# Kernel tuning notes

Measured on AMD Instinct MI355X. Metric: run time of the kernel, lower is better.

## Reference

```python
import jax, jax.numpy as jnp
import numpy as np

B, IN, OUT, ORDER = 8192, 1024, 1024, 7


def setup_inputs() -> dict:
    key = jax.random.key(0)
    k1, k2 = jax.random.split(key)
    x = jax.random.normal(k1, (B, IN), dtype=jnp.float32)
    tanh_range = jnp.float32(1.0)
    coef = jax.random.normal(k2, (OUT, IN, ORDER + 1), dtype=jnp.float32) * 0.1
    return {"x": x, "tanh_range": tanh_range, "coef": coef}


def _poly(x, tanh_range, order):
    # t^0, t^1, ..., t^order via cumulative products (matches torch recurrence)
    t = jnp.tanh(x * tanh_range)                      # [B, IN]
    powers = jnp.cumprod(jnp.broadcast_to(t[..., None], t.shape + (order,)), axis=-1)
    ones = jnp.ones_like(t)[..., None]
    return jnp.concatenate([ones, powers], axis=-1)   # [B, IN, order+1]


def reference(x, tanh_range, coef):
    poly = _poly(x, tanh_range, ORDER)                # [B, IN, K]
    # output[b, j] = sum_{i,k} coef[j,i,k] * poly[b,i,k]
    return jnp.einsum('bik,jik->bj', poly, coef)
```

## Files before the change

### kernel.cpp

```cpp
#include <hip/hip_runtime.h>
#include <hip/hip_bf16.h>


#define BM 128
#define BN 128
#define BK 128
#define KT 7168
#define KFULL 8192

typedef short bf16x8 __attribute__((ext_vector_type(8)));
typedef short bf16x4 __attribute__((ext_vector_type(4)));
typedef float f32x4  __attribute__((ext_vector_type(4)));

__device__ __forceinline__ unsigned short f2bf(float f) {
    union { float f; unsigned u; } v; v.f = f;
    unsigned r = v.u + 0x7fffu + ((v.u >> 16) & 1u);
    return (unsigned short)(r >> 16);
}

__device__ __forceinline__ void gload_lds16(const void* gp, void* lp) {
    __builtin_amdgcn_global_load_lds(
        (const __attribute__((address_space(1))) void*)gp,
        (__attribute__((address_space(3))) void*)lp, 16, 0, 0);
}

#define CVT_BLOCKS  512
#define TANH_BLOCKS 4096

__global__ __launch_bounds__(256)
void prep(const float* __restrict__ x, const float* __restrict__ trp,
          const float* __restrict__ coef, unsigned short* __restrict__ coef_bf,
          unsigned short* __restrict__ A, float* __restrict__ bias) {
    __shared__ unsigned short st[256 * 56];
    __shared__ float redbuf[4];

    const int t   = threadIdx.x;
    const int blk = blockIdx.x;
    const int rl  = t >> 7;
    const int ig  = t & 127;
    const bool is_cvt = (blk < CVT_BLOCKS);

    unsigned short tmp[56];

    if (is_cvt) {
        const int j = blk * 2 + rl;
        const float* src = coef + (size_t)j * KFULL + ig * 64;
        float k0sum = 0.f;
        #pragma unroll
        for (int i = 0; i < 8; ++i) {
            const float4 f0 = *(const float4*)(src + i * 8);
            const float4 f1 = *(const float4*)(src + i * 8 + 4);
            k0sum += f0.x;
            tmp[i*7+0] = f2bf(f0.y); tmp[i*7+1] = f2bf(f0.z); tmp[i*7+2] = f2bf(f0.w);
            tmp[i*7+3] = f2bf(f1.x); tmp[i*7+4] = f2bf(f1.y);
            tmp[i*7+5] = f2bf(f1.z); tmp[i*7+6] = f2bf(f1.w);
        }
        #pragma unroll
        for (int off = 32; off > 0; off >>= 1) k0sum += __shfl_down(k0sum, off, 64);
        if ((t & 63) == 0) redbuf[t >> 6] = k0sum;
    } else {
        const int bb = (blk - CVT_BLOCKS) * 2 + rl;
        const float tr = trp[0];
        const float* xp = x + (size_t)bb * 1024 + ig * 8;
        const float4 x0 = *(const float4*)xp;
        const float4 x1 = *(const float4*)(xp + 4);
        const float xs[8] = {x0.x, x0.y, x0.z, x0.w, x1.x, x1.y, x1.z, x1.w};
        #pragma unroll
        for (int i = 0; i < 8; ++i) {
            const float e  = __expf(2.0f * tr * xs[i]);
            const float tt = 1.0f - 2.0f * __builtin_amdgcn_rcpf(e + 1.0f);
            float pw = tt;
            #pragma unroll
            for (int k = 1; k < 8; ++k) { tmp[i * 7 + k - 1] = f2bf(pw); pw *= tt; }
        }
    }

    #pragma unroll
    for (int v = 0; v < 7; ++v)
        *(bf16x8*)&st[t * 56 + v * 8] = *(bf16x8*)&tmp[v * 8];

    __syncthreads();

    if (is_cvt) {
        if (t == 0)   bias[blk * 2]     = redbuf[0] + redbuf[1];
        if (t == 128) bias[blk * 2 + 1] = redbuf[2] + redbuf[3];
    }

    unsigned short* dstbase = is_cvt
        ? coef_bf + (size_t)(blk * 2) * KT
        : A       + (size_t)((blk - CVT_BLOCKS) * 2) * KT;
    #pragma unroll
    for (int v = 0; v < 7; ++v) {
        const int c   = v * 256 + t;
        const int row = c / 896;
        const int cc  = c - row * 896;
        const int igs = cc / 7;
        const int q   = cc - igs * 7;
        const bf16x8 pk = *(const bf16x8*)&st[(row * 128 + igs) * 56 + q * 8];
        *(bf16x8*)(dstbase + (size_t)c * 8) = pk;
    }
}

__global__ __launch_bounds__(256, 2)
void gemm_bt(const unsigned short* __restrict__ A, const unsigned short* __restrict__ Bt,
             const float* __restrict__ bias, float* __restrict__ out)
{
    __shared__ unsigned short As[BM * BK];
    __shared__ unsigned short Bs[BN * BK];

    const int t    = threadIdx.x;
    const int m0   = blockIdx.x * BM;
    const int n0   = blockIdx.y * BN;
    const int w    = t >> 6;
    const int lane = t & 63;
    const int wm   = (w >> 1) * 64;
    const int wn   = (w & 1) * 64;
    const int lrow = lane & 15;

    const int srow   = t >> 4;
    const int schunk = (t & 15) ^ srow;
    const int wbase  = w * 512;

    f32x4 acc[4][4];
    #pragma unroll
    for (int i = 0; i < 4; i++)
        #pragma unroll
        for (int j = 0; j < 4; j++)
            acc[i][j] = (f32x4){0.f, 0.f, 0.f, 0.f};

    const size_t abase = (size_t)(m0 + srow) * KT + schunk * 8;
    const size_t bbase = (size_t)(n0 + srow) * KT + schunk * 8;

    for (int k0 = 0; k0 < KT; k0 += BK) {
        #pragma unroll
        for (int r = 0; r < 8; ++r)
            gload_lds16(A + abase + (size_t)r * 16 * KT + k0, &As[r * 2048 + wbase]);
        #pragma unroll
        for (int r = 0; r < 8; ++r)
            gload_lds16(Bt + bbase + (size_t)r * 16 * KT + k0, &Bs[r * 2048 + wbase]);

        __syncthreads();

        #pragma unroll
        for (int kk = 0; kk < BK; kk += 32) {
            const int soff = ((((kk >> 3) + (lane >> 4)) ^ (lane & 15)) * 8);
            bf16x8 a[4], b[4];
            #pragma unroll
            for (int i = 0; i < 4; i++)
                a[i] = *(const bf16x8*)&As[(wm + i * 16 + lrow) * BK + soff];
            #pragma unroll
            for (int j = 0; j < 4; j++)
                b[j] = *(const bf16x8*)&Bs[(wn + j * 16 + lrow) * BK + soff];
            #pragma unroll
            for (int i = 0; i < 4; i++)
                #pragma unroll
                for (int j = 0; j < 4; j++)
                    acc[i][j] = __builtin_amdgcn_mfma_f32_16x16x32_bf16(a[i], b[j], acc[i][j], 0, 0, 0);
        }

        __syncthreads();
    }

    const int crow = (lane >> 4) * 4;
    const int ccol = lane & 15;
    #pragma unroll
    for (int j = 0; j < 4; j++) {
        const int n = n0 + wn + j * 16 + ccol;
        const float bv = bias[n];
        #pragma unroll
        for (int i = 0; i < 4; i++) {
            const int m = m0 + wm + i * 16 + crow;
            #pragma unroll
            for (int r = 0; r < 4; ++r)
                out[(size_t)(m + r) * 1024 + n] = acc[i][j][r] + bv;
        }
    }
}

#define LDK 72
__global__ __launch_bounds__(256, 2)
void taylor_gemm(const float* __restrict__ x, const float* __restrict__ trp,
                 const float* __restrict__ coef, float* __restrict__ out)
{
    __shared__ unsigned short As[BM * LDK];
    __shared__ unsigned short Bs[BN * LDK];

    const int t  = threadIdx.x;
    const int m0 = blockIdx.x * BM;
    const int n0 = blockIdx.y * BN;
    const float tr = trp[0];

    const int w    = t >> 6;
    const int lane = t & 63;
    const int wm   = (w >> 1) * 64;
    const int wn   = (w & 1) * 64;
    const int lrow = lane & 15;
    const int kq   = (lane >> 4) * 8;

    f32x4 acc[4][4];
    #pragma unroll
    for (int i = 0; i < 4; i++)
        #pragma unroll
        for (int j = 0; j < 4; j++)
            acc[i][j] = (f32x4){0.f, 0.f, 0.f, 0.f};

    const int bcol  = t & 15;
    const int brow0 = t >> 4;
    const int acol  = t & 7;
    const int arow0 = t >> 3;

    for (int k0 = 0; k0 < KFULL; k0 += 64) {
        const int i0 = k0 >> 3;
        #pragma unroll
        for (int r = 0; r < 8; ++r) {
            const int row = brow0 + r * 16;
            const float4 v = *(const float4*)(coef + (size_t)(n0 + row) * KFULL + k0 + bcol * 4);
            bf16x4 pk;
            pk[0] = (short)f2bf(v.x); pk[1] = (short)f2bf(v.y);
            pk[2] = (short)f2bf(v.z); pk[3] = (short)f2bf(v.w);
            *(bf16x4*)&Bs[row * LDK + bcol * 4] = pk;
        }
        #pragma unroll
        for (int r = 0; r < 4; ++r) {
            const int row = arow0 + r * 32;
            const float xv = x[(size_t)(m0 + row) * 1024 + i0 + acol];
            const float e  = __expf(2.0f * tr * xv);
            const float tt = 1.0f - 2.0f / (e + 1.0f);
            bf16x8 pk;
            float p = 1.0f;
            #pragma unroll
            for (int k = 0; k < 8; ++k) { pk[k] = (short)f2bf(p); p *= tt; }
            *(bf16x8*)&As[row * LDK + acol * 8] = pk;
        }
        __syncthreads();
        #pragma unroll
        for (int kk = 0; kk < 64; kk += 32) {
            bf16x8 a[4], b[4];
            #pragma unroll
            for (int i = 0; i < 4; i++)
                a[i] = *(const bf16x8*)&As[(wm + i * 16 + lrow) * LDK + kk + kq];
            #pragma unroll
            for (int j = 0; j < 4; j++)
                b[j] = *(const bf16x8*)&Bs[(wn + j * 16 + lrow) * LDK + kk + kq];
            #pragma unroll
            for (int i = 0; i < 4; i++)
                #pragma unroll
                for (int j = 0; j < 4; j++)
                    acc[i][j] = __builtin_amdgcn_mfma_f32_16x16x32_bf16(a[i], b[j], acc[i][j], 0, 0, 0);
        }
        __syncthreads();
    }

    const int crow = (lane >> 4) * 4;
    const int ccol = lane & 15;
    #pragma unroll
    for (int i = 0; i < 4; i++) {
        #pragma unroll
        for (int j = 0; j < 4; j++) {
            const int m = m0 + wm + i * 16 + crow;
            const int n = n0 + wn + j * 16 + ccol;
            #pragma unroll
            for (int r = 0; r < 4; ++r)
                out[(size_t)(m + r) * 1024 + n] = acc[i][j][r];
        }
    }
}

extern "C" void kernel_launch(void* const* d_in, const int* in_sizes, int n_in,
                              void* d_out, int out_size, void* d_ws, size_t ws_size,
                              hipStream_t stream) {
    const float* x    = (const float*)d_in[0];
    const float* trp  = (const float*)d_in[1];
    const float* coef = (const float*)d_in[2];
    float* out = (float*)d_out;

    const size_t A_BYTES    = (size_t)8192 * KT * 2;
    const size_t COEF_BYTES = (size_t)1024 * KT * 2;
    const size_t BIAS_BYTES = 1024 * sizeof(float);
    dim3 block(256);

    if (ws_size >= A_BYTES + COEF_BYTES + BIAS_BYTES) {
        unsigned short* A_bf    = (unsigned short*)d_ws;
        unsigned short* coef_bf = (unsigned short*)((char*)d_ws + A_BYTES);
        float*          bias    = (float*)((char*)d_ws + A_BYTES + COEF_BYTES);

        prep<<<dim3(CVT_BLOCKS + TANH_BLOCKS), block, 0, stream>>>(
            x, trp, coef, coef_bf, A_bf, bias);
        gemm_bt<<<dim3(8192 / BM, 1024 / BN), block, 0, stream>>>(
            A_bf, coef_bf, bias, out);
    } else {
        taylor_gemm<<<dim3(8192 / BM, 1024 / BN), block, 0, stream>>>(x, trp, coef, out);
    }
}
```

Measured before the change: 229.3 us.

## Rewrite bf16 GEMM with 256x128 tiles, triple-buffered async loads and split barriers

```diff
diff --git a/kernel.cpp b/kernel.cpp
--- a/kernel.cpp
+++ b/kernel.cpp
@@ -2,11 +2,18 @@
 #include <hip/hip_bf16.h>
 
 
+#define KT 7168
+#define KFULL 8192
+
+#define TM 256
+#define TN 128
+#define TK 64
+#define NTILES (KT / TK)
+#define BUF_USH 24576
+#define BOFF 16384
+
 #define BM 128
 #define BN 128
-#define BK 128
-#define KT 7168
-#define KFULL 8192
 
 typedef short bf16x8 __attribute__((ext_vector_type(8)));
 typedef short bf16x4 __attribute__((ext_vector_type(4)));
@@ -23,6 +30,12 @@
         (const __attribute__((address_space(1))) void*)gp,
         (__attribute__((address_space(3))) void*)lp, 16, 0, 0);
 }
+
+#define BARRIER() do { \
+    asm volatile("" ::: "memory"); \
+    __builtin_amdgcn_s_barrier(); \
+    asm volatile("" ::: "memory"); \
+} while (0)
 
 #define CVT_BLOCKS  512
 #define TANH_BLOCKS 4096
@@ -101,25 +114,29 @@
     }
 }
 
-__global__ __launch_bounds__(256, 2)
+__global__ __launch_bounds__(512, 2)
 void gemm_bt(const unsigned short* __restrict__ A, const unsigned short* __restrict__ Bt,
              const float* __restrict__ bias, float* __restrict__ out)
 {
-    __shared__ unsigned short As[BM * BK];
-    __shared__ unsigned short Bs[BN * BK];
+    __shared__ unsigned short lds[3 * BUF_USH];
 
     const int t    = threadIdx.x;
-    const int m0   = blockIdx.x * BM;
-    const int n0   = blockIdx.y * BN;
+    const int m0   = blockIdx.x * TM;
+    const int n0   = blockIdx.y * TN;
     const int w    = t >> 6;
     const int lane = t & 63;
     const int wm   = (w >> 1) * 64;
     const int wn   = (w & 1) * 64;
     const int lrow = lane & 15;
-
-    const int srow   = t >> 4;
-    const int schunk = (t & 15) ^ srow;
-    const int wbase  = w * 512;
+    const int lq   = lane >> 4;
+
+    const int S = ((lq ^ (lane & 7)) << 3);
+
+    const int srow = t >> 3;
+    const int schk = (t & 7) ^ (srow & 7);
+    const size_t aGbase = (size_t)(m0 + srow) * KT + schk * 8;
+    const size_t bGbase = (size_t)(n0 + srow) * KT + schk * 8;
+    const int wofs = w * 512;
 
     f32x4 acc[4][4];
     #pragma unroll
@@ -128,37 +145,97 @@
         for (int j = 0; j < 4; j++)
             acc[i][j] = (f32x4){0.f, 0.f, 0.f, 0.f};
 
-    const size_t abase = (size_t)(m0 + srow) * KT + schunk * 8;
-    const size_t bbase = (size_t)(n0 + srow) * KT + schunk * 8;
-
-    for (int k0 = 0; k0 < KT; k0 += BK) {
-        #pragma unroll
-        for (int r = 0; r < 8; ++r)
-            gload_lds16(A + abase + (size_t)r * 16 * KT + k0, &As[r * 2048 + wbase]);
-        #pragma unroll
-        for (int r = 0; r < 8; ++r)
-            gload_lds16(Bt + bbase + (size_t)r * 16 * KT + k0, &Bs[r * 2048 + wbase]);
-
-        __syncthreads();
-
-        #pragma unroll
-        for (int kk = 0; kk < BK; kk += 32) {
-            const int soff = ((((kk >> 3) + (lane >> 4)) ^ (lane & 15)) * 8);
-            bf16x8 a[4], b[4];
-            #pragma unroll
-            for (int i = 0; i < 4; i++)
-                a[i] = *(const bf16x8*)&As[(wm + i * 16 + lrow) * BK + soff];
-            #pragma unroll
-            for (int j = 0; j < 4; j++)
-                b[j] = *(const bf16x8*)&Bs[(wn + j * 16 + lrow) * BK + soff];
-            #pragma unroll
-            for (int i = 0; i < 4; i++)
+    #pragma unroll
+    for (int s = 0; s < 4; ++s)
+        gload_lds16(A + aGbase + (size_t)(s * 64) * KT, &lds[s * 4096 + wofs]);
+    #pragma unroll
+    for (int s = 0; s < 2; ++s)
+        gload_lds16(Bt + bGbase + (size_t)(s * 64) * KT, &lds[BOFF + s * 4096 + wofs]);
+    #pragma unroll
+    for (int s = 0; s < 4; ++s)
+        gload_lds16(A + aGbase + (size_t)(s * 64) * KT + TK, &lds[BUF_USH + s * 4096 + wofs]);
+    #pragma unroll
+    for (int s = 0; s < 2; ++s)
+        gload_lds16(Bt + bGbase + (size_t)(s * 64) * KT + TK, &lds[BUF_USH + BOFF + s * 4096 + wofs]);
+
+    asm volatile("s_waitcnt vmcnt(6)" ::: "memory");
+    BARRIER();
+
+    int bufR = 0;
+    int bufW = 2 * BUF_USH;
+
+    for (int kt = 0; kt < NTILES; ++kt) {
+        const int  k2 = (kt + 2) * TK;
+        const bool pf = (kt + 2 < NTILES);
+
+        bf16x8 b0[4][2], a0[2][2];
+        #pragma unroll
+        for (int j = 0; j < 4; ++j) {
+            const int base = bufR + BOFF + (wn + j * 16 + lrow) * 64 + S;
+            b0[j][0] = *(const bf16x8*)&lds[base];
+            b0[j][1] = *(const bf16x8*)&lds[base ^ 32];
+        }
+        #pragma unroll
+        for (int i = 0; i < 2; ++i) {
+            const int base = bufR + (wm + i * 16 + lrow) * 64 + S;
+            a0[i][0] = *(const bf16x8*)&lds[base];
+            a0[i][1] = *(const bf16x8*)&lds[base ^ 32];
+        }
+        if (pf) {
+            #pragma unroll
+            for (int s = 0; s < 3; ++s)
+                gload_lds16(A + aGbase + (size_t)(s * 64) * KT + k2,
+                            &lds[bufW + s * 4096 + wofs]);
+        }
+        BARRIER();
+        __builtin_amdgcn_s_setprio(1);
+        #pragma unroll
+        for (int kk = 0; kk < 2; ++kk)
+            #pragma unroll
+            for (int i = 0; i < 2; ++i)
                 #pragma unroll
-                for (int j = 0; j < 4; j++)
-                    acc[i][j] = __builtin_amdgcn_mfma_f32_16x16x32_bf16(a[i], b[j], acc[i][j], 0, 0, 0);
-        }
-
-        __syncthreads();
+                for (int j = 0; j < 4; ++j)
+                    acc[i][j] = __builtin_amdgcn_mfma_f32_16x16x32_bf16(
+                        a0[i][kk], b0[j][kk], acc[i][j], 0, 0, 0);
+        __builtin_amdgcn_s_setprio(0);
+        BARRIER();
+
+        bf16x8 a1[2][2];
+        #pragma unroll
+        for (int i = 0; i < 2; ++i) {
+            const int base = bufR + (wm + (i + 2) * 16 + lrow) * 64 + S;
+            a1[i][0] = *(const bf16x8*)&lds[base];
+            a1[i][1] = *(const bf16x8*)&lds[base ^ 32];
+        }
+        if (pf) {
+            gload_lds16(A + aGbase + (size_t)(3 * 64) * KT + k2,
+                        &lds[bufW + 3 * 4096 + wofs]);
+            #pragma unroll
+            for (int s = 0; s < 2; ++s)
+                gload_lds16(Bt + bGbase + (size_t)(s * 64) * KT + k2,
+                            &lds[bufW + BOFF + s * 4096 + wofs]);
+        }
+        BARRIER();
+        __builtin_amdgcn_s_setprio(1);
+        #pragma unroll
+        for (int kk = 0; kk < 2; ++kk)
+            #pragma unroll
+            for (int i = 0; i < 2; ++i)
+                #pragma unroll
+                for (int j = 0; j < 4; ++j)
+                    acc[i + 2][j] = __builtin_amdgcn_mfma_f32_16x16x32_bf16(
+                        a1[i][kk], b0[j][kk], acc[i + 2][j], 0, 0, 0);
+        __builtin_amdgcn_s_setprio(0);
+
+        if (kt < NTILES - 2) {
+            asm volatile("s_waitcnt vmcnt(6)" ::: "memory");
+        } else if (kt == NTILES - 2) {
+            asm volatile("s_waitcnt vmcnt(0)" ::: "memory");
+        }
+        BARRIER();
+
+        bufR += BUF_USH; if (bufR == 3 * BUF_USH) bufR = 0;
+        bufW += BUF_USH; if (bufW == 3 * BUF_USH) bufW = 0;
     }
 
     const int crow = (lane >> 4) * 4;
@@ -277,18 +354,17 @@
     const size_t A_BYTES    = (size_t)8192 * KT * 2;
     const size_t COEF_BYTES = (size_t)1024 * KT * 2;
     const size_t BIAS_BYTES = 1024 * sizeof(float);
-    dim3 block(256);
 
     if (ws_size >= A_BYTES + COEF_BYTES + BIAS_BYTES) {
         unsigned short* A_bf    = (unsigned short*)d_ws;
         unsigned short* coef_bf = (unsigned short*)((char*)d_ws + A_BYTES);
         float*          bias    = (float*)((char*)d_ws + A_BYTES + COEF_BYTES);
 
-        prep<<<dim3(CVT_BLOCKS + TANH_BLOCKS), block, 0, stream>>>(
+        prep<<<dim3(CVT_BLOCKS + TANH_BLOCKS), dim3(256), 0, stream>>>(
             x, trp, coef, coef_bf, A_bf, bias);
-        gemm_bt<<<dim3(8192 / BM, 1024 / BN), block, 0, stream>>>(
+        gemm_bt<<<dim3(8192 / TM, 1024 / TN), dim3(512), 0, stream>>>(
             A_bf, coef_bf, bias, out);
     } else {
-        taylor_gemm<<<dim3(8192 / BM, 1024 / BN), block, 0, stream>>>(x, trp, coef, out);
-    }
-}
+        taylor_gemm<<<dim3(8192 / BM, 1024 / BN), dim3(256), 0, stream>>>(x, trp, coef, out);
+    }
+}
```

Result: slower. 238.5 us (+4.0%).

## Double-buffer GEMM LDS tiles and write planar bf16 operands directly from prep

Applied to the files above, without the earlier changes.

```diff
diff --git a/kernel.cpp b/kernel.cpp
--- a/kernel.cpp
+++ b/kernel.cpp
@@ -2,11 +2,16 @@
 #include <hip/hip_bf16.h>
 
 
+#define KT 7168
+#define KFULL 8192
+
+#define TM 128
+#define TN 128
+#define TK 64
+#define NT (KT / TK)
+
 #define BM 128
 #define BN 128
-#define BK 128
-#define KT 7168
-#define KFULL 8192
 
 typedef short bf16x8 __attribute__((ext_vector_type(8)));
 typedef short bf16x4 __attribute__((ext_vector_type(4)));
@@ -31,33 +36,39 @@
 void prep(const float* __restrict__ x, const float* __restrict__ trp,
           const float* __restrict__ coef, unsigned short* __restrict__ coef_bf,
           unsigned short* __restrict__ A, float* __restrict__ bias) {
-    __shared__ unsigned short st[256 * 56];
     __shared__ float redbuf[4];
 
     const int t   = threadIdx.x;
     const int blk = blockIdx.x;
     const int rl  = t >> 7;
     const int ig  = t & 127;
-    const bool is_cvt = (blk < CVT_BLOCKS);
-
-    unsigned short tmp[56];
-
-    if (is_cvt) {
+
+    if (blk < CVT_BLOCKS) {
         const int j = blk * 2 + rl;
         const float* src = coef + (size_t)j * KFULL + ig * 64;
         float k0sum = 0.f;
+        bf16x8 pl[7];
         #pragma unroll
         for (int i = 0; i < 8; ++i) {
             const float4 f0 = *(const float4*)(src + i * 8);
             const float4 f1 = *(const float4*)(src + i * 8 + 4);
             k0sum += f0.x;
-            tmp[i*7+0] = f2bf(f0.y); tmp[i*7+1] = f2bf(f0.z); tmp[i*7+2] = f2bf(f0.w);
-            tmp[i*7+3] = f2bf(f1.x); tmp[i*7+4] = f2bf(f1.y);
-            tmp[i*7+5] = f2bf(f1.z); tmp[i*7+6] = f2bf(f1.w);
+            pl[0][i] = (short)f2bf(f0.y); pl[1][i] = (short)f2bf(f0.z);
+            pl[2][i] = (short)f2bf(f0.w); pl[3][i] = (short)f2bf(f1.x);
+            pl[4][i] = (short)f2bf(f1.y); pl[5][i] = (short)f2bf(f1.z);
+            pl[6][i] = (short)f2bf(f1.w);
         }
         #pragma unroll
         for (int off = 32; off > 0; off >>= 1) k0sum += __shfl_down(k0sum, off, 64);
         if ((t & 63) == 0) redbuf[t >> 6] = k0sum;
+        __syncthreads();
+        if (t == 0)   bias[j]     = redbuf[0] + redbuf[1];
+        if (t == 128) bias[j]     = redbuf[2] + redbuf[3];
+
+        unsigned short* dst = coef_bf + (size_t)j * KT + ig * 8;
+        #pragma unroll
+        for (int p = 0; p < 7; ++p)
+            *(bf16x8*)(dst + p * 1024) = pl[p];
     } else {
         const int bb = (blk - CVT_BLOCKS) * 2 + rl;
         const float tr = trp[0];
@@ -65,39 +76,19 @@
         const float4 x0 = *(const float4*)xp;
         const float4 x1 = *(const float4*)(xp + 4);
         const float xs[8] = {x0.x, x0.y, x0.z, x0.w, x1.x, x1.y, x1.z, x1.w};
+        bf16x8 pl[7];
         #pragma unroll
         for (int i = 0; i < 8; ++i) {
             const float e  = __expf(2.0f * tr * xs[i]);
             const float tt = 1.0f - 2.0f * __builtin_amdgcn_rcpf(e + 1.0f);
             float pw = tt;
             #pragma unroll
-            for (int k = 1; k < 8; ++k) { tmp[i * 7 + k - 1] = f2bf(pw); pw *= tt; }
-        }
-    }
-
-    #pragma unroll
-    for (int v = 0; v < 7; ++v)
-        *(bf16x8*)&st[t * 56 + v * 8] = *(bf16x8*)&tmp[v * 8];
-
-    __syncthreads();
-
-    if (is_cvt) {
-        if (t == 0)   bias[blk * 2]     = redbuf[0] + redbuf[1];
-        if (t == 128) bias[blk * 2 + 1] = redbuf[2] + redbuf[3];
-    }
-
-    unsigned short* dstbase = is_cvt
-        ? coef_bf + (size_t)(blk * 2) * KT
-        : A       + (size_t)((blk - CVT_BLOCKS) * 2) * KT;
-    #pragma unroll
-    for (int v = 0; v < 7; ++v) {
-        const int c   = v * 256 + t;
-        const int row = c / 896;
-        const int cc  = c - row * 896;
-        const int igs = cc / 7;
-        const int q   = cc - igs * 7;
-        const bf16x8 pk = *(const bf16x8*)&st[(row * 128 + igs) * 56 + q * 8];
-        *(bf16x8*)(dstbase + (size_t)c * 8) = pk;
+            for (int p = 0; p < 7; ++p) { pl[p][i] = (short)f2bf(pw); pw *= tt; }
+        }
+        unsigned short* dst = A + (size_t)bb * KT + ig * 8;
+        #pragma unroll
+        for (int p = 0; p < 7; ++p)
+            *(bf16x8*)(dst + p * 1024) = pl[p];
     }
 }
 
@@ -105,21 +96,26 @@
 void gemm_bt(const unsigned short* __restrict__ A, const unsigned short* __restrict__ Bt,
              const float* __restrict__ bias, float* __restrict__ out)
 {
-    __shared__ unsigned short As[BM * BK];
-    __shared__ unsigned short Bs[BN * BK];
+    __shared__ unsigned short As[2][TM * TK];
+    __shared__ unsigned short Bs[2][TN * TK];
 
     const int t    = threadIdx.x;
-    const int m0   = blockIdx.x * BM;
-    const int n0   = blockIdx.y * BN;
+    const int m0   = blockIdx.x * TM;
+    const int n0   = blockIdx.y * TN;
     const int w    = t >> 6;
     const int lane = t & 63;
     const int wm   = (w >> 1) * 64;
     const int wn   = (w & 1) * 64;
     const int lrow = lane & 15;
-
-    const int srow   = t >> 4;
-    const int schunk = (t & 15) ^ srow;
-    const int wbase  = w * 512;
+    const int lq   = lane >> 4;
+
+    const int S = ((lq ^ (lane & 7)) << 3);
+
+    const int srow = t >> 3;
+    const int schk = (t & 7) ^ (srow & 7);
+    const size_t aG = (size_t)(m0 + srow) * KT + schk * 8;
+    const size_t bG = (size_t)(n0 + srow) * KT + schk * 8;
+    const int wofs = w * 512;
 
     f32x4 acc[4][4];
     #pragma unroll
@@ -128,35 +124,48 @@
         for (int j = 0; j < 4; j++)
             acc[i][j] = (f32x4){0.f, 0.f, 0.f, 0.f};
 
-    const size_t abase = (size_t)(m0 + srow) * KT + schunk * 8;
-    const size_t bbase = (size_t)(n0 + srow) * KT + schunk * 8;
-
-    for (int k0 = 0; k0 < KT; k0 += BK) {
-        #pragma unroll
-        for (int r = 0; r < 8; ++r)
-            gload_lds16(A + abase + (size_t)r * 16 * KT + k0, &As[r * 2048 + wbase]);
-        #pragma unroll
-        for (int r = 0; r < 8; ++r)
-            gload_lds16(Bt + bbase + (size_t)r * 16 * KT + k0, &Bs[r * 2048 + wbase]);
-
-        __syncthreads();
-
-        #pragma unroll
-        for (int kk = 0; kk < BK; kk += 32) {
-            const int soff = ((((kk >> 3) + (lane >> 4)) ^ (lane & 15)) * 8);
-            bf16x8 a[4], b[4];
-            #pragma unroll
-            for (int i = 0; i < 4; i++)
-                a[i] = *(const bf16x8*)&As[(wm + i * 16 + lrow) * BK + soff];
-            #pragma unroll
-            for (int j = 0; j < 4; j++)
-                b[j] = *(const bf16x8*)&Bs[(wn + j * 16 + lrow) * BK + soff];
-            #pragma unroll
-            for (int i = 0; i < 4; i++)
+    #pragma unroll
+    for (int r = 0; r < 4; ++r) {
+        gload_lds16(A  + aG + (size_t)(r * 32) * KT, &As[0][r * 2048 + wofs]);
+        gload_lds16(Bt + bG + (size_t)(r * 32) * KT, &Bs[0][r * 2048 + wofs]);
+    }
+    __syncthreads();
+
+    for (int kt = 0; kt < NT; ++kt) {
+        const int cur = kt & 1;
+
+        if (kt + 1 < NT) {
+            const size_t ko = (size_t)(kt + 1) * TK;
+            #pragma unroll
+            for (int r = 0; r < 4; ++r) {
+                gload_lds16(A  + aG + (size_t)(r * 32) * KT + ko, &As[cur ^ 1][r * 2048 + wofs]);
+                gload_lds16(Bt + bG + (size_t)(r * 32) * KT + ko, &Bs[cur ^ 1][r * 2048 + wofs]);
+            }
+        }
+
+        const unsigned short* as = As[cur];
+        const unsigned short* bs = Bs[cur];
+        bf16x8 a[2][4], b[2][4];
+        #pragma unroll
+        for (int i = 0; i < 4; ++i) {
+            const int ro = (wm + i * 16 + lrow) * TK + S;
+            a[0][i] = *(const bf16x8*)&as[ro];
+            a[1][i] = *(const bf16x8*)&as[ro ^ 32];
+        }
+        #pragma unroll
+        for (int j = 0; j < 4; ++j) {
+            const int ro = (wn + j * 16 + lrow) * TK + S;
+            b[0][j] = *(const bf16x8*)&bs[ro];
+            b[1][j] = *(const bf16x8*)&bs[ro ^ 32];
+        }
+        #pragma unroll
+        for (int kk = 0; kk < 2; ++kk)
+            #pragma unroll
+            for (int i = 0; i < 4; ++i)
                 #pragma unroll
-                for (int j = 0; j < 4; j++)
-                    acc[i][j] = __builtin_amdgcn_mfma_f32_16x16x32_bf16(a[i], b[j], acc[i][j], 0, 0, 0);
-        }
+                for (int j = 0; j < 4; ++j)
+                    acc[i][j] = __builtin_amdgcn_mfma_f32_16x16x32_bf16(
+                        a[kk][i], b[kk][j], acc[i][j], 0, 0, 0);
 
         __syncthreads();
     }
@@ -277,18 +286,17 @@
     const size_t A_BYTES    = (size_t)8192 * KT * 2;
     const size_t COEF_BYTES = (size_t)1024 * KT * 2;
     const size_t BIAS_BYTES = 1024 * sizeof(float);
-    dim3 block(256);
 
     if (ws_size >= A_BYTES + COEF_BYTES + BIAS_BYTES) {
         unsigned short* A_bf    = (unsigned short*)d_ws;
         unsigned short* coef_bf = (unsigned short*)((char*)d_ws + A_BYTES);
         float*          bias    = (float*)((char*)d_ws + A_BYTES + COEF_BYTES);
 
-        prep<<<dim3(CVT_BLOCKS + TANH_BLOCKS), block, 0, stream>>>(
+        prep<<<dim3(CVT_BLOCKS + TANH_BLOCKS), dim3(256), 0, stream>>>(
             x, trp, coef, coef_bf, A_bf, bias);
-        gemm_bt<<<dim3(8192 / BM, 1024 / BN), block, 0, stream>>>(
+        gemm_bt<<<dim3(8192 / TM, 1024 / TN), dim3(256), 0, stream>>>(
             A_bf, coef_bf, bias, out);
     } else {
-        taylor_gemm<<<dim3(8192 / BM, 1024 / BN), block, 0, stream>>>(x, trp, coef, out);
-    }
-}
+        taylor_gemm<<<dim3(8192 / BM, 1024 / BN), dim3(256), 0, stream>>>(x, trp, coef, out);
+    }
+}
```

Result: slower. 239.1 us (+4.3%).
